# Performance work log

Hardware: AMD Instinct MI355X
Metric: run time of the kernel (lower is better)

Reference implementation:

```python
import jax, jax.numpy as jnp
import numpy as np

N_NODES = 50000

def _gcn_conv(x, W, b, src, dst, n):
    # GCNConv: add self-loops, symmetric normalization D^-1/2 (A+I) D^-1/2, then aggregate X@W
    h = x @ W  # [N, out]
    loop = jnp.arange(n, dtype=src.dtype)
    s = jnp.concatenate([src, loop])
    d = jnp.concatenate([dst, loop])
    deg = jax.ops.segment_sum(jnp.ones_like(d, dtype=h.dtype), d, num_segments=n)  # in-degree incl self-loop (>=1)
    dinv = jax.lax.rsqrt(deg)
    norm = dinv[s] * dinv[d]  # [E+N]
    msg = h[s] * norm[:, None]  # gather + scale
    out = jax.ops.segment_sum(msg, d, num_segments=n)  # scatter-add
    return out + b

def setup_inputs() -> dict:
    key = jax.random.key(0)
    k1, k2, k3, k4, k5 = jax.random.split(key, 5)
    F_IN, HID, CLS, E = 256, 128, 32, 800000
    x = jax.random.normal(k1, (N_NODES, F_IN), dtype=jnp.float32)
    edge_index = jax.random.randint(k2, (2, E), 0, N_NODES, dtype=jnp.int64)
    W1 = jax.random.normal(k3, (F_IN, HID), dtype=jnp.float32) / np.sqrt(F_IN)
    b1 = jnp.zeros((HID,), dtype=jnp.float32)
    W2 = jax.random.normal(k4, (HID, CLS), dtype=jnp.float32) / np.sqrt(HID)
    b2 = jnp.zeros((CLS,), dtype=jnp.float32)
    return {"x": x, "edge_index": edge_index, "W1": W1, "b1": b1, "W2": W2, "b2": b2}

def reference(x, edge_index, W1, b1, W2, b2):
    src, dst = edge_index[0], edge_index[1]
    h = _gcn_conv(x, W1, b1, src, dst, N_NODES)
    h = jax.nn.relu(h)
    h = _gcn_conv(h, W2, b2, src, dst, N_NODES)
    return jax.nn.log_softmax(h, axis=1)
```

## Files before the change

kernel.cpp:

```cpp
#include <hip/hip_runtime.h>

#define N_NODES 50000
#define N_PAD   50176
#define F_IN 256
#define HID 128
#define CLS 32
#define N_EDGE 800000

#define NB    196
#define NPART 196
#define CHUNK 4082

typedef short bf16x8 __attribute__((ext_vector_type(8)));
typedef short s16x8  __attribute__((ext_vector_type(8)));
typedef float f32x2  __attribute__((ext_vector_type(2)));
typedef float f32x4  __attribute__((ext_vector_type(4)));
typedef float f32x8  __attribute__((ext_vector_type(8)));

static __device__ inline short f2bf(float f) {
    union { float f; unsigned u; } v; v.f = f;
    unsigned r = v.u + 0x7FFFu + ((v.u >> 16) & 1u);
    return (short)(r >> 16);
}

static __device__ inline unsigned char f2fp8(float f) {
    return (unsigned char)(__builtin_amdgcn_cvt_pk_fp8_f32(f, f, 0, false) & 0xFF);
}


__global__ __launch_bounds__(256) void k_pre(const int* __restrict__ dst,
                                             int* __restrict__ counts,
                                             const float* __restrict__ W1,
                                             short* __restrict__ Wt,
                                             const float* __restrict__ W2,
                                             short* __restrict__ Wt2) {
    int blk = blockIdx.x, tid = threadIdx.x;
    if (blk < NB) {
        __shared__ int hist[NPART];
        if (tid < NPART) hist[tid] = 0;
        __syncthreads();
        int lo = blk * CHUNK, hi = min(lo + CHUNK, N_EDGE);
        for (int e = lo + tid; e < hi; e += 256)
            atomicAdd(&hist[dst[e] >> 8], 1);
        __syncthreads();
        if (tid < NPART) counts[blk * NPART + tid] = hist[tid];
    } else if (blk < NB + 128) {
        int idx = (blk - NB) * 256 + tid;
        int k = idx >> 7;
        int n = idx & 127;
        Wt[n * F_IN + k] = f2bf(W1[(size_t)k * HID + n]);
    } else {
        int idx = (blk - NB - 128) * 256 + tid;
        int k = idx >> 5;
        int n = idx & 31;
        Wt2[n * HID + k] = f2bf(W2[(size_t)k * CLS + n]);
    }
}


__global__ __launch_bounds__(256) void k_scanP1(const int* __restrict__ counts,
                                                int* __restrict__ base,
                                                int* __restrict__ ptot) {
    __shared__ int s[256];
    int tid = threadIdx.x, p = blockIdx.x;
    int v = (tid < NB) ? counts[tid * NPART + p] : 0;
    s[tid] = v;
    __syncthreads();
#pragma unroll
    for (int off = 1; off < 256; off <<= 1) {
        int t = (tid >= off) ? s[tid - off] : 0;
        __syncthreads();
        s[tid] += t;
        __syncthreads();
    }
    if (tid < NB) base[tid * NPART + p] = s[tid] - v;
    if (tid == 255) ptot[p] = s[255];
}


__global__ __launch_bounds__(256) void k_bucket(const int* __restrict__ src,
                                                const int* __restrict__ dst,
                                                const int* __restrict__ base,
                                                const int* __restrict__ ptot,
                                                int* __restrict__ bucket) {
    __shared__ int s[256];
    __shared__ int cur[NPART];
    int tid = threadIdx.x, blk = blockIdx.x;
    int v = (tid < NPART) ? ptot[tid] : 0;
    s[tid] = v;
    __syncthreads();
#pragma unroll
    for (int off = 1; off < 256; off <<= 1) {
        int t = (tid >= off) ? s[tid - off] : 0;
        __syncthreads();
        s[tid] += t;
        __syncthreads();
    }
    if (tid < NPART) cur[tid] = base[blk * NPART + tid] + (s[tid] - v);
    __syncthreads();
    int lo = blk * CHUNK, hi = min(lo + CHUNK, N_EDGE);
    for (int e = lo + tid; e < hi; e += 256) {
        int d = dst[e], sv = src[e];
        int pos = atomicAdd(&cur[d >> 8], 1);
        bucket[pos] = ((d & 255) << 16) | sv;
    }
}


__global__ __launch_bounds__(256) void k_csrf_gemm1(const int* __restrict__ bucket,
                                                    const int* __restrict__ ptot,
                                                    int* __restrict__ esrc,
                                                    int* __restrict__ offs,
                                                    float* __restrict__ dinv,
                                                    const float* __restrict__ x,
                                                    const short* __restrict__ Wt,
                                                    unsigned char* __restrict__ h) {
    int blk = blockIdx.x, tid = threadIdx.x;
    if (blk < NPART) {
        __shared__ int s[256], hist[256], cur[256];
        __shared__ int sbeg;
        int p = blk;
        int v = (tid < NPART) ? ptot[tid] : 0;
        s[tid] = v;
        __syncthreads();
#pragma unroll
        for (int off = 1; off < 256; off <<= 1) {
            int t = (tid >= off) ? s[tid - off] : 0;
            __syncthreads();
            s[tid] += t;
            __syncthreads();
        }
        if (tid == p) sbeg = s[tid] - v;
        hist[tid] = 0;
        __syncthreads();
        int beg = sbeg, end = sbeg + ptot[p];
        for (int i = beg + tid; i < end; i += 256)
            atomicAdd(&hist[bucket[i] >> 16], 1);
        __syncthreads();
        int hv = hist[tid];
        s[tid] = hv;
        __syncthreads();
#pragma unroll
        for (int off = 1; off < 256; off <<= 1) {
            int t = (tid >= off) ? s[tid - off] : 0;
            __syncthreads();
            s[tid] += t;
            __syncthreads();
        }
        int excl = s[tid] - hv;
        cur[tid] = excl;
        int node = p * 256 + tid;
        if (node <= N_NODES) offs[node] = beg + excl;
        if (node < N_NODES) dinv[node] = rsqrtf((float)(hv + 1));
        __syncthreads();
        for (int i = beg + tid; i < end; i += 256) {
            int pk = bucket[i];
            int slot = atomicAdd(&cur[pk >> 16], 1);
            esrc[beg + slot] = pk & 0xFFFF;
        }
        return;
    }

    const int gblk = blk - NPART;
    const int lane = tid & 63;
    const int w    = tid >> 6;
    const int l15  = lane & 15;
    const int lk   = lane >> 4;
    const int row0 = gblk * 128 + w * 32;

    f32x4 acc[2][8] = {};

#pragma unroll
    for (int ks = 0; ks < F_IN / 32; ++ks) {
        const int kbase = ks * 32 + lk * 8;

        bf16x8 afrag[2];
#pragma unroll
        for (int mt = 0; mt < 2; ++mt) {
            int row = row0 + mt * 16 + l15;
            row = min(row, N_NODES - 1);
            f32x8 xv = *(const f32x8*)(x + (size_t)row * F_IN + kbase);
            bf16x8 a;
#pragma unroll
            for (int e = 0; e < 8; ++e) a[e] = f2bf(xv[e]);
            afrag[mt] = a;
        }

        bf16x8 bfrag[8];
#pragma unroll
        for (int nt = 0; nt < 8; ++nt) {
            int col = nt * 16 + l15;
            bfrag[nt] = *(const bf16x8*)(Wt + (size_t)col * F_IN + kbase);
        }

#pragma unroll
        for (int mt = 0; mt < 2; ++mt)
#pragma unroll
            for (int nt = 0; nt < 8; ++nt)
                acc[mt][nt] = __builtin_amdgcn_mfma_f32_16x16x32_bf16(
                    afrag[mt], bfrag[nt], acc[mt][nt], 0, 0, 0);
    }

#pragma unroll
    for (int mt = 0; mt < 2; ++mt) {
#pragma unroll
        for (int r = 0; r < 4; ++r) {
            int m = row0 + mt * 16 + lk * 4 + r;
            if (m < N_NODES) {
#pragma unroll
                for (int nt = 0; nt < 8; ++nt) {
                    int n = nt * 16 + l15;
                    h[(size_t)m * HID + n] = f2fp8(acc[mt][nt][r]);
                }
            }
        }
    }
}


__global__ __launch_bounds__(256) void k_gather1(const int* __restrict__ offs,
                                                 const int* __restrict__ esrc,
                                                 const unsigned char* __restrict__ h,
                                                 const float* __restrict__ dinv,
                                                 const float* __restrict__ b,
                                                 short* __restrict__ out) {
    int node = blockIdx.x * 16 + (threadIdx.x >> 4);
    int lane = threadIdx.x & 15;
    if (node >= N_NODES) return;
    int f = lane * 8;
    float dv = dinv[node];
    uint2 hv = *(const uint2*)(h + (size_t)node * HID + f);
    f32x2 q0 = __builtin_amdgcn_cvt_pk_f32_fp8(hv.x, false);
    f32x2 q1 = __builtin_amdgcn_cvt_pk_f32_fp8(hv.x, true);
    f32x2 q2 = __builtin_amdgcn_cvt_pk_f32_fp8(hv.y, false);
    f32x2 q3 = __builtin_amdgcn_cvt_pk_f32_fp8(hv.y, true);
    float self = dv * dv;
    float a0 = q0[0] * self, a1 = q0[1] * self, a2 = q1[0] * self, a3 = q1[1] * self;
    float a4 = q2[0] * self, a5 = q2[1] * self, a6 = q3[0] * self, a7 = q3[1] * self;

    int beg = offs[node], end = offs[node + 1];
    int p = beg;
#define ACC8(vv, nn) { \
    f32x2 c0 = __builtin_amdgcn_cvt_pk_f32_fp8(vv.x, false); \
    f32x2 c1 = __builtin_amdgcn_cvt_pk_f32_fp8(vv.x, true);  \
    f32x2 c2 = __builtin_amdgcn_cvt_pk_f32_fp8(vv.y, false); \
    f32x2 c3 = __builtin_amdgcn_cvt_pk_f32_fp8(vv.y, true);  \
    a0 += c0[0] * nn; a1 += c0[1] * nn; a2 += c1[0] * nn; a3 += c1[1] * nn; \
    a4 += c2[0] * nn; a5 += c2[1] * nn; a6 += c3[0] * nn; a7 += c3[1] * nn; }
    for (; p + 7 < end; p += 8) {
        int s0 = esrc[p + 0], s1 = esrc[p + 1], s2 = esrc[p + 2], s3 = esrc[p + 3];
        int s4 = esrc[p + 4], s5 = esrc[p + 5], s6 = esrc[p + 6], s7 = esrc[p + 7];
        float n0 = dinv[s0] * dv, n1 = dinv[s1] * dv, n2 = dinv[s2] * dv, n3 = dinv[s3] * dv;
        float n4 = dinv[s4] * dv, n5 = dinv[s5] * dv, n6 = dinv[s6] * dv, n7 = dinv[s7] * dv;
        uint2 v0 = *(const uint2*)(h + (size_t)s0 * HID + f);
        uint2 v1 = *(const uint2*)(h + (size_t)s1 * HID + f);
        uint2 v2 = *(const uint2*)(h + (size_t)s2 * HID + f);
        uint2 v3 = *(const uint2*)(h + (size_t)s3 * HID + f);
        uint2 v4 = *(const uint2*)(h + (size_t)s4 * HID + f);
        uint2 v5 = *(const uint2*)(h + (size_t)s5 * HID + f);
        uint2 v6 = *(const uint2*)(h + (size_t)s6 * HID + f);
        uint2 v7 = *(const uint2*)(h + (size_t)s7 * HID + f);
        ACC8(v0, n0); ACC8(v1, n1); ACC8(v2, n2); ACC8(v3, n3);
        ACC8(v4, n4); ACC8(v5, n5); ACC8(v6, n6); ACC8(v7, n7);
    }
    for (; p + 3 < end; p += 4) {
        int s0 = esrc[p + 0], s1 = esrc[p + 1], s2 = esrc[p + 2], s3 = esrc[p + 3];
        float n0 = dinv[s0] * dv, n1 = dinv[s1] * dv, n2 = dinv[s2] * dv, n3 = dinv[s3] * dv;
        uint2 v0 = *(const uint2*)(h + (size_t)s0 * HID + f);
        uint2 v1 = *(const uint2*)(h + (size_t)s1 * HID + f);
        uint2 v2 = *(const uint2*)(h + (size_t)s2 * HID + f);
        uint2 v3 = *(const uint2*)(h + (size_t)s3 * HID + f);
        ACC8(v0, n0); ACC8(v1, n1); ACC8(v2, n2); ACC8(v3, n3);
    }
    for (; p < end; ++p) {
        int s = esrc[p];
        float nrm = dinv[s] * dv;
        uint2 v = *(const uint2*)(h + (size_t)s * HID + f);
        ACC8(v, nrm);
    }
#undef ACC8
    float4 bv0 = *(const float4*)(b + f);
    float4 bv1 = *(const float4*)(b + f + 4);
    s16x8 o = { f2bf(a0 + bv0.x), f2bf(a1 + bv0.y), f2bf(a2 + bv0.z), f2bf(a3 + bv0.w),
                f2bf(a4 + bv1.x), f2bf(a5 + bv1.y), f2bf(a6 + bv1.z), f2bf(a7 + bv1.w) };
    *(s16x8*)(out + (size_t)node * HID + f) = o;
}


__global__ __launch_bounds__(256) void k_gemm2_mfma(const short* __restrict__ a,
                                                    const short* __restrict__ Wt,
                                                    unsigned char* __restrict__ h) {
    const int lane = threadIdx.x & 63;
    const int w    = threadIdx.x >> 6;
    const int l15  = lane & 15;
    const int lk   = lane >> 4;
    const int row0 = blockIdx.x * 128 + w * 32;

    f32x4 acc[2][2] = {};

#pragma unroll
    for (int ks = 0; ks < HID / 32; ++ks) {
        const int kbase = ks * 32 + lk * 8;

        bf16x8 afrag[2];
#pragma unroll
        for (int mt = 0; mt < 2; ++mt) {
            int row = row0 + mt * 16 + l15;
            row = min(row, N_NODES - 1);
            bf16x8 av = *(const bf16x8*)(a + (size_t)row * HID + kbase);
#pragma unroll
            for (int e = 0; e < 8; ++e) if (av[e] < 0) av[e] = 0;
            afrag[mt] = av;
        }

        bf16x8 bfrag[2];
#pragma unroll
        for (int nt = 0; nt < 2; ++nt) {
            int col = nt * 16 + l15;
            bfrag[nt] = *(const bf16x8*)(Wt + (size_t)col * HID + kbase);
        }

#pragma unroll
        for (int mt = 0; mt < 2; ++mt)
#pragma unroll
            for (int nt = 0; nt < 2; ++nt)
                acc[mt][nt] = __builtin_amdgcn_mfma_f32_16x16x32_bf16(
                    afrag[mt], bfrag[nt], acc[mt][nt], 0, 0, 0);
    }

#pragma unroll
    for (int mt = 0; mt < 2; ++mt) {
#pragma unroll
        for (int r = 0; r < 4; ++r) {
            int m = row0 + mt * 16 + lk * 4 + r;
            if (m < N_NODES) {
#pragma unroll
                for (int nt = 0; nt < 2; ++nt) {
                    int n = nt * 16 + l15;
                    h[(size_t)m * CLS + n] = f2fp8(acc[mt][nt][r]);
                }
            }
        }
    }
}


__global__ __launch_bounds__(256) void k_gather2(const int* __restrict__ offs,
                                                 const int* __restrict__ esrc,
                                                 const unsigned char* __restrict__ h,
                                                 const float* __restrict__ dinv,
                                                 const float* __restrict__ b,
                                                 float* __restrict__ out) {
    int node = blockIdx.x * 32 + (threadIdx.x >> 3);
    int sub = threadIdx.x & 7;
    if (node >= N_NODES) return;
    int f = sub * 4;
    float dv = dinv[node];
    unsigned hv = *(const unsigned*)(h + (size_t)node * CLS + f);
    f32x2 hlo = __builtin_amdgcn_cvt_pk_f32_fp8(hv, false);
    f32x2 hhi = __builtin_amdgcn_cvt_pk_f32_fp8(hv, true);
    float self = dv * dv;
    float a0 = hlo[0] * self, a1 = hlo[1] * self, a2 = hhi[0] * self, a3 = hhi[1] * self;
    int beg = offs[node], end = offs[node + 1];
    int p = beg;
#define ACC4(vv, nn) { \
    f32x2 l = __builtin_amdgcn_cvt_pk_f32_fp8(vv, false); \
    f32x2 u = __builtin_amdgcn_cvt_pk_f32_fp8(vv, true);  \
    a0 += l[0] * nn; a1 += l[1] * nn; a2 += u[0] * nn; a3 += u[1] * nn; }
    for (; p + 7 < end; p += 8) {
        int s0 = esrc[p], s1 = esrc[p + 1], s2 = esrc[p + 2], s3 = esrc[p + 3];
        int s4 = esrc[p + 4], s5 = esrc[p + 5], s6 = esrc[p + 6], s7 = esrc[p + 7];
        float n0 = dinv[s0] * dv, n1 = dinv[s1] * dv, n2 = dinv[s2] * dv, n3 = dinv[s3] * dv;
        float n4 = dinv[s4] * dv, n5 = dinv[s5] * dv, n6 = dinv[s6] * dv, n7 = dinv[s7] * dv;
        unsigned v0 = *(const unsigned*)(h + (size_t)s0 * CLS + f);
        unsigned v1 = *(const unsigned*)(h + (size_t)s1 * CLS + f);
        unsigned v2 = *(const unsigned*)(h + (size_t)s2 * CLS + f);
        unsigned v3 = *(const unsigned*)(h + (size_t)s3 * CLS + f);
        unsigned v4 = *(const unsigned*)(h + (size_t)s4 * CLS + f);
        unsigned v5 = *(const unsigned*)(h + (size_t)s5 * CLS + f);
        unsigned v6 = *(const unsigned*)(h + (size_t)s6 * CLS + f);
        unsigned v7 = *(const unsigned*)(h + (size_t)s7 * CLS + f);
        ACC4(v0, n0); ACC4(v1, n1); ACC4(v2, n2); ACC4(v3, n3);
        ACC4(v4, n4); ACC4(v5, n5); ACC4(v6, n6); ACC4(v7, n7);
    }
    for (; p + 3 < end; p += 4) {
        int s0 = esrc[p], s1 = esrc[p + 1], s2 = esrc[p + 2], s3 = esrc[p + 3];
        float n0 = dinv[s0] * dv, n1 = dinv[s1] * dv, n2 = dinv[s2] * dv, n3 = dinv[s3] * dv;
        unsigned v0 = *(const unsigned*)(h + (size_t)s0 * CLS + f);
        unsigned v1 = *(const unsigned*)(h + (size_t)s1 * CLS + f);
        unsigned v2 = *(const unsigned*)(h + (size_t)s2 * CLS + f);
        unsigned v3 = *(const unsigned*)(h + (size_t)s3 * CLS + f);
        ACC4(v0, n0); ACC4(v1, n1); ACC4(v2, n2); ACC4(v3, n3);
    }
    for (; p < end; ++p) {
        int s = esrc[p];
        float nrm = dinv[s] * dv;
        unsigned v = *(const unsigned*)(h + (size_t)s * CLS + f);
        ACC4(v, nrm);
    }
#undef ACC4
    float4 bv = *(const float4*)(b + f);
    float4 acc = { a0 + bv.x, a1 + bv.y, a2 + bv.z, a3 + bv.w };

    float m = fmaxf(fmaxf(acc.x, acc.y), fmaxf(acc.z, acc.w));
    m = fmaxf(m, __shfl_xor(m, 1, 8));
    m = fmaxf(m, __shfl_xor(m, 2, 8));
    m = fmaxf(m, __shfl_xor(m, 4, 8));
    float sum = expf(acc.x - m) + expf(acc.y - m) + expf(acc.z - m) + expf(acc.w - m);
    sum += __shfl_xor(sum, 1, 8);
    sum += __shfl_xor(sum, 2, 8);
    sum += __shfl_xor(sum, 4, 8);
    float l = m + logf(sum);
    float4 o = { acc.x - l, acc.y - l, acc.z - l, acc.w - l };
    *(float4*)(out + (size_t)node * CLS + f) = o;
}


extern "C" void kernel_launch(void* const* d_in, const int* in_sizes, int n_in,
                              void* d_out, int out_size, void* d_ws, size_t ws_size,
                              hipStream_t stream) {
    const float* x  = (const float*)d_in[0];
    const int*   ei = (const int*)d_in[1];
    const float* W1 = (const float*)d_in[2];
    const float* b1 = (const float*)d_in[3];
    const float* W2 = (const float*)d_in[4];
    const float* b2 = (const float*)d_in[5];
    float* out = (float*)d_out;

    const int* src = ei;
    const int* dst = ei + N_EDGE;

    int* counts   = (int*)d_ws;
    int* base     = counts + NB * NPART;
    int* ptot     = base + NB * NPART;
    int* bucket   = ptot + 256;
    int* offs     = bucket + N_EDGE;
    int* esrc     = offs + N_PAD;
    float* dinv   = (float*)(esrc + N_EDGE);
    unsigned char* h1 = (unsigned char*)(dinv + N_PAD);
    short* a1     = (short*)(h1 + (size_t)N_NODES * HID);
    unsigned char* h2 = (unsigned char*)(a1 + (size_t)N_NODES * HID);
    short* Wt     = (short*)(h2 + (size_t)N_NODES * CLS);
    short* Wt2    = Wt + HID * F_IN;

    k_pre       <<<NB + 128 + 16, 256, 0, stream>>>(dst, counts, W1, Wt, W2, Wt2);
    k_scanP1    <<<NPART,         256, 0, stream>>>(counts, base, ptot);
    k_bucket    <<<NB,            256, 0, stream>>>(src, dst, base, ptot, bucket);
    k_csrf_gemm1<<<NPART + 391,   256, 0, stream>>>(bucket, ptot, esrc, offs, dinv, x, Wt, h1);

    k_gather1   <<<3125,          256, 0, stream>>>(offs, esrc, h1, dinv, b1, a1);
    k_gemm2_mfma<<<391,           256, 0, stream>>>(a1, Wt2, h2);
    k_gather2   <<<1563,          256, 0, stream>>>(offs, esrc, h2, dinv, b2, out);
}
```

Measured before the change: 92.18 us.

## Co-schedule GEMM1 with edge bucketing and shrink GEMM tile to 64 rows

The first feature GEMM now runs in the same launch as the edge-bucketing step instead of alongside the CSR finalization, and CSR finalization becomes its own kernel. The intent is to hide the long bucketing scatter behind GEMM work, with a lighter CSR kernel afterward. The GEMM tile also drops from 128 to 64 rows per block (782 blocks), which cuts register use and spreads the work over more blocks. The cost is that each B fragment is reused across fewer rows, so W is reloaded more often.

Result: slower. 105.5 us (+14.4%).

```diff
diff --git a/kernel.cpp b/kernel.cpp
--- a/kernel.cpp
+++ b/kernel.cpp
@@ -10,6 +10,7 @@
 #define NB    196
 #define NPART 196
 #define CHUNK 4082
+#define GBLKS 782
 
 typedef short bf16x8 __attribute__((ext_vector_type(8)));
 typedef short s16x8  __attribute__((ext_vector_type(8)));
@@ -78,48 +79,18 @@
 }
 
 
-__global__ __launch_bounds__(256) void k_bucket(const int* __restrict__ src,
-                                                const int* __restrict__ dst,
-                                                const int* __restrict__ base,
-                                                const int* __restrict__ ptot,
-                                                int* __restrict__ bucket) {
-    __shared__ int s[256];
-    __shared__ int cur[NPART];
-    int tid = threadIdx.x, blk = blockIdx.x;
-    int v = (tid < NPART) ? ptot[tid] : 0;
-    s[tid] = v;
-    __syncthreads();
-#pragma unroll
-    for (int off = 1; off < 256; off <<= 1) {
-        int t = (tid >= off) ? s[tid - off] : 0;
-        __syncthreads();
-        s[tid] += t;
-        __syncthreads();
-    }
-    if (tid < NPART) cur[tid] = base[blk * NPART + tid] + (s[tid] - v);
-    __syncthreads();
-    int lo = blk * CHUNK, hi = min(lo + CHUNK, N_EDGE);
-    for (int e = lo + tid; e < hi; e += 256) {
-        int d = dst[e], sv = src[e];
-        int pos = atomicAdd(&cur[d >> 8], 1);
-        bucket[pos] = ((d & 255) << 16) | sv;
-    }
-}
-
-
-__global__ __launch_bounds__(256) void k_csrf_gemm1(const int* __restrict__ bucket,
-                                                    const int* __restrict__ ptot,
-                                                    int* __restrict__ esrc,
-                                                    int* __restrict__ offs,
-                                                    float* __restrict__ dinv,
-                                                    const float* __restrict__ x,
-                                                    const short* __restrict__ Wt,
-                                                    unsigned char* __restrict__ h) {
+__global__ __launch_bounds__(256) void k_bucket_gemm1(const int* __restrict__ src,
+                                                      const int* __restrict__ dst,
+                                                      const int* __restrict__ base,
+                                                      const int* __restrict__ ptot,
+                                                      int* __restrict__ bucket,
+                                                      const float* __restrict__ x,
+                                                      const short* __restrict__ Wt,
+                                                      unsigned char* __restrict__ h) {
     int blk = blockIdx.x, tid = threadIdx.x;
-    if (blk < NPART) {
-        __shared__ int s[256], hist[256], cur[256];
-        __shared__ int sbeg;
-        int p = blk;
+    if (blk < NB) {
+        __shared__ int s[256];
+        __shared__ int cur[NPART];
         int v = (tid < NPART) ? ptot[tid] : 0;
         s[tid] = v;
         __syncthreads();
@@ -130,61 +101,35 @@
             s[tid] += t;
             __syncthreads();
         }
-        if (tid == p) sbeg = s[tid] - v;
-        hist[tid] = 0;
-        __syncthreads();
-        int beg = sbeg, end = sbeg + ptot[p];
-        for (int i = beg + tid; i < end; i += 256)
-            atomicAdd(&hist[bucket[i] >> 16], 1);
-        __syncthreads();
-        int hv = hist[tid];
-        s[tid] = hv;
-        __syncthreads();
-#pragma unroll
-        for (int off = 1; off < 256; off <<= 1) {
-            int t = (tid >= off) ? s[tid - off] : 0;
-            __syncthreads();
-            s[tid] += t;
-            __syncthreads();
-        }
-        int excl = s[tid] - hv;
-        cur[tid] = excl;
-        int node = p * 256 + tid;
-        if (node <= N_NODES) offs[node] = beg + excl;
-        if (node < N_NODES) dinv[node] = rsqrtf((float)(hv + 1));
-        __syncthreads();
-        for (int i = beg + tid; i < end; i += 256) {
-            int pk = bucket[i];
-            int slot = atomicAdd(&cur[pk >> 16], 1);
-            esrc[beg + slot] = pk & 0xFFFF;
+        if (tid < NPART) cur[tid] = base[blk * NPART + tid] + (s[tid] - v);
+        __syncthreads();
+        int lo = blk * CHUNK, hi = min(lo + CHUNK, N_EDGE);
+        for (int e = lo + tid; e < hi; e += 256) {
+            int d = dst[e], sv = src[e];
+            int pos = atomicAdd(&cur[d >> 8], 1);
+            bucket[pos] = ((d & 255) << 16) | sv;
         }
         return;
     }
 
-    const int gblk = blk - NPART;
+    const int gblk = blk - NB;
     const int lane = tid & 63;
     const int w    = tid >> 6;
     const int l15  = lane & 15;
     const int lk   = lane >> 4;
-    const int row0 = gblk * 128 + w * 32;
-
-    f32x4 acc[2][8] = {};
+    const int row0 = gblk * 64 + w * 16;
+
+    f32x4 acc[8] = {};
 
 #pragma unroll
     for (int ks = 0; ks < F_IN / 32; ++ks) {
         const int kbase = ks * 32 + lk * 8;
 
-        bf16x8 afrag[2];
-#pragma unroll
-        for (int mt = 0; mt < 2; ++mt) {
-            int row = row0 + mt * 16 + l15;
-            row = min(row, N_NODES - 1);
-            f32x8 xv = *(const f32x8*)(x + (size_t)row * F_IN + kbase);
-            bf16x8 a;
-#pragma unroll
-            for (int e = 0; e < 8; ++e) a[e] = f2bf(xv[e]);
-            afrag[mt] = a;
-        }
+        int row = min(row0 + l15, N_NODES - 1);
+        f32x8 xv = *(const f32x8*)(x + (size_t)row * F_IN + kbase);
+        bf16x8 afrag;
+#pragma unroll
+        for (int e = 0; e < 8; ++e) afrag[e] = f2bf(xv[e]);
 
         bf16x8 bfrag[8];
 #pragma unroll
@@ -194,26 +139,69 @@
         }
 
 #pragma unroll
-        for (int mt = 0; mt < 2; ++mt)
-#pragma unroll
-            for (int nt = 0; nt < 8; ++nt)
-                acc[mt][nt] = __builtin_amdgcn_mfma_f32_16x16x32_bf16(
-                    afrag[mt], bfrag[nt], acc[mt][nt], 0, 0, 0);
-    }
-
-#pragma unroll
-    for (int mt = 0; mt < 2; ++mt) {
-#pragma unroll
-        for (int r = 0; r < 4; ++r) {
-            int m = row0 + mt * 16 + lk * 4 + r;
-            if (m < N_NODES) {
-#pragma unroll
-                for (int nt = 0; nt < 8; ++nt) {
-                    int n = nt * 16 + l15;
-                    h[(size_t)m * HID + n] = f2fp8(acc[mt][nt][r]);
-                }
+        for (int nt = 0; nt < 8; ++nt)
+            acc[nt] = __builtin_amdgcn_mfma_f32_16x16x32_bf16(afrag, bfrag[nt], acc[nt], 0, 0, 0);
+    }
+
+#pragma unroll
+    for (int r = 0; r < 4; ++r) {
+        int m = row0 + lk * 4 + r;
+        if (m < N_NODES) {
+#pragma unroll
+            for (int nt = 0; nt < 8; ++nt) {
+                int n = nt * 16 + l15;
+                h[(size_t)m * HID + n] = f2fp8(acc[nt][r]);
             }
         }
+    }
+}
+
+
+__global__ __launch_bounds__(256) void k_csr_final(const int* __restrict__ bucket,
+                                                   const int* __restrict__ ptot,
+                                                   int* __restrict__ esrc,
+                                                   int* __restrict__ offs,
+                                                   float* __restrict__ dinv) {
+    __shared__ int s[256], hist[256], cur[256];
+    __shared__ int sbeg;
+    int tid = threadIdx.x, p = blockIdx.x;
+    int v = (tid < NPART) ? ptot[tid] : 0;
+    s[tid] = v;
+    __syncthreads();
+#pragma unroll
+    for (int off = 1; off < 256; off <<= 1) {
+        int t = (tid >= off) ? s[tid - off] : 0;
+        __syncthreads();
+        s[tid] += t;
+        __syncthreads();
+    }
+    if (tid == p) sbeg = s[tid] - v;
+    hist[tid] = 0;
+    __syncthreads();
+    int beg = sbeg, end = sbeg + ptot[p];
+    for (int i = beg + tid; i < end; i += 256)
+        atomicAdd(&hist[bucket[i] >> 16], 1);
+    __syncthreads();
+    int hv = hist[tid];
+    s[tid] = hv;
+    __syncthreads();
+#pragma unroll
+    for (int off = 1; off < 256; off <<= 1) {
+        int t = (tid >= off) ? s[tid - off] : 0;
+        __syncthreads();
+        s[tid] += t;
+        __syncthreads();
+    }
+    int excl = s[tid] - hv;
+    cur[tid] = excl;
+    int node = p * 256 + tid;
+    if (node <= N_NODES) offs[node] = beg + excl;
+    if (node < N_NODES) dinv[node] = rsqrtf((float)(hv + 1));
+    __syncthreads();
+    for (int i = beg + tid; i < end; i += 256) {
+        int pk = bucket[i];
+        int slot = atomicAdd(&cur[pk >> 16], 1);
+        esrc[beg + slot] = pk & 0xFFFF;
     }
 }
 
@@ -443,12 +431,12 @@
     short* Wt     = (short*)(h2 + (size_t)N_NODES * CLS);
     short* Wt2    = Wt + HID * F_IN;
 
-    k_pre       <<<NB + 128 + 16, 256, 0, stream>>>(dst, counts, W1, Wt, W2, Wt2);
-    k_scanP1    <<<NPART,         256, 0, stream>>>(counts, base, ptot);
-    k_bucket    <<<NB,            256, 0, stream>>>(src, dst, base, ptot, bucket);
-    k_csrf_gemm1<<<NPART + 391,   256, 0, stream>>>(bucket, ptot, esrc, offs, dinv, x, Wt, h1);
-
-    k_gather1   <<<3125,          256, 0, stream>>>(offs, esrc, h1, dinv, b1, a1);
-    k_gemm2_mfma<<<391,           256, 0, stream>>>(a1, Wt2, h2);
-    k_gather2   <<<1563,          256, 0, stream>>>(offs, esrc, h2, dinv, b2, out);
-}
+    k_pre         <<<NB + 128 + 16, 256, 0, stream>>>(dst, counts, W1, Wt, W2, Wt2);
+    k_scanP1      <<<NPART,         256, 0, stream>>>(counts, base, ptot);
+    k_bucket_gemm1<<<NB + GBLKS,    256, 0, stream>>>(src, dst, base, ptot, bucket, x, Wt, h1);
+    k_csr_final   <<<NPART,         256, 0, stream>>>(bucket, ptot, esrc, offs, dinv);
+
+    k_gather1     <<<3125,          256, 0, stream>>>(offs, esrc, h1, dinv, b1, a1);
+    k_gemm2_mfma  <<<391,           256, 0, stream>>>(a1, Wt2, h2);
+    k_gather2     <<<1563,          256, 0, stream>>>(offs, esrc, h2, dinv, b2, out);
+}
```

## Stage X tile through swizzled LDS and halve rows per GEMM1 block

Applied to the files above, without the earlier changes.

The GEMM1 part of the fused CSR/GEMM kernel now loads a 64-row tile of x into shared memory with coalesced float4 loads, converts it to bf16, and stores it with an XOR swizzle. MFMA A-fragments are then read from LDS. Each wave now handles 16 rows instead of 32, so the grid doubles to 782 GEMM blocks for more parallelism. The cost is a 32KB LDS allocation for every block, including the CSR blocks that reuse it, which can lower occupancy. Each W fragment is also reused across fewer rows, so more B loads happen per output.

Result: slower. 101.0 us (+9.6%).

```diff
diff --git a/kernel.cpp b/kernel.cpp
--- a/kernel.cpp
+++ b/kernel.cpp
@@ -10,12 +10,13 @@
 #define NB    196
 #define NPART 196
 #define CHUNK 4082
+#define GBLKS 782
 
 typedef short bf16x8 __attribute__((ext_vector_type(8)));
+typedef short s16x4  __attribute__((ext_vector_type(4)));
 typedef short s16x8  __attribute__((ext_vector_type(8)));
 typedef float f32x2  __attribute__((ext_vector_type(2)));
 typedef float f32x4  __attribute__((ext_vector_type(4)));
-typedef float f32x8  __attribute__((ext_vector_type(8)));
 
 static __device__ inline short f2bf(float f) {
     union { float f; unsigned u; } v; v.f = f;
@@ -115,76 +116,86 @@
                                                     const float* __restrict__ x,
                                                     const short* __restrict__ Wt,
                                                     unsigned char* __restrict__ h) {
+    __shared__ short tile[64][256];
     int blk = blockIdx.x, tid = threadIdx.x;
+
     if (blk < NPART) {
-        __shared__ int s[256], hist[256], cur[256];
-        __shared__ int sbeg;
+        int* sA = (int*)&tile[0][0];
+        int* sB = sA + 256;
+        int* sC = sB + 256;
+        int* sX = sC + 256;
         int p = blk;
         int v = (tid < NPART) ? ptot[tid] : 0;
-        s[tid] = v;
+        sA[tid] = v;
         __syncthreads();
 #pragma unroll
         for (int off = 1; off < 256; off <<= 1) {
-            int t = (tid >= off) ? s[tid - off] : 0;
+            int t = (tid >= off) ? sA[tid - off] : 0;
             __syncthreads();
-            s[tid] += t;
+            sA[tid] += t;
             __syncthreads();
         }
-        if (tid == p) sbeg = s[tid] - v;
-        hist[tid] = 0;
-        __syncthreads();
-        int beg = sbeg, end = sbeg + ptot[p];
+        if (tid == p) sX[0] = sA[tid] - v;
+        sB[tid] = 0;
+        __syncthreads();
+        int beg = sX[0], end = beg + ptot[p];
         for (int i = beg + tid; i < end; i += 256)
-            atomicAdd(&hist[bucket[i] >> 16], 1);
-        __syncthreads();
-        int hv = hist[tid];
-        s[tid] = hv;
+            atomicAdd(&sB[bucket[i] >> 16], 1);
+        __syncthreads();
+        int hv = sB[tid];
+        sA[tid] = hv;
         __syncthreads();
 #pragma unroll
         for (int off = 1; off < 256; off <<= 1) {
-            int t = (tid >= off) ? s[tid - off] : 0;
+            int t = (tid >= off) ? sA[tid - off] : 0;
             __syncthreads();
-            s[tid] += t;
+            sA[tid] += t;
             __syncthreads();
         }
-        int excl = s[tid] - hv;
-        cur[tid] = excl;
+        int excl = sA[tid] - hv;
+        sC[tid] = excl;
         int node = p * 256 + tid;
         if (node <= N_NODES) offs[node] = beg + excl;
         if (node < N_NODES) dinv[node] = rsqrtf((float)(hv + 1));
         __syncthreads();
         for (int i = beg + tid; i < end; i += 256) {
             int pk = bucket[i];
-            int slot = atomicAdd(&cur[pk >> 16], 1);
+            int slot = atomicAdd(&sC[pk >> 16], 1);
             esrc[beg + slot] = pk & 0xFFFF;
         }
         return;
     }
 
-    const int gblk = blk - NPART;
+    const int R0 = (blk - NPART) * 64;
+
+#pragma unroll 8
+    for (int it = 0; it < 16; ++it) {
+        int rl = it * 4 + (tid >> 6);
+        int row = min(R0 + rl, N_NODES - 1);
+        int c = (tid & 63) * 4;
+        f32x4 xv = *(const f32x4*)(x + (size_t)row * F_IN + c);
+        s16x4 bv = { f2bf(xv[0]), f2bf(xv[1]), f2bf(xv[2]), f2bf(xv[3]) };
+        int byte = rl * 512 + c * 2;
+        byte ^= ((rl & 7) << 4);
+        *(s16x4*)((char*)&tile[0][0] + byte) = bv;
+    }
+    __syncthreads();
+
     const int lane = tid & 63;
     const int w    = tid >> 6;
     const int l15  = lane & 15;
     const int lk   = lane >> 4;
-    const int row0 = gblk * 128 + w * 32;
-
-    f32x4 acc[2][8] = {};
+
+    f32x4 acc[8] = {};
 
 #pragma unroll
     for (int ks = 0; ks < F_IN / 32; ++ks) {
         const int kbase = ks * 32 + lk * 8;
 
-        bf16x8 afrag[2];
-#pragma unroll
-        for (int mt = 0; mt < 2; ++mt) {
-            int row = row0 + mt * 16 + l15;
-            row = min(row, N_NODES - 1);
-            f32x8 xv = *(const f32x8*)(x + (size_t)row * F_IN + kbase);
-            bf16x8 a;
-#pragma unroll
-            for (int e = 0; e < 8; ++e) a[e] = f2bf(xv[e]);
-            afrag[mt] = a;
-        }
+        int rl = w * 16 + l15;
+        int byte = rl * 512 + kbase * 2;
+        byte ^= ((rl & 7) << 4);
+        bf16x8 afrag = *(const bf16x8*)((char*)&tile[0][0] + byte);
 
         bf16x8 bfrag[8];
 #pragma unroll
@@ -194,24 +205,18 @@
         }
 
 #pragma unroll
-        for (int mt = 0; mt < 2; ++mt)
-#pragma unroll
-            for (int nt = 0; nt < 8; ++nt)
-                acc[mt][nt] = __builtin_amdgcn_mfma_f32_16x16x32_bf16(
-                    afrag[mt], bfrag[nt], acc[mt][nt], 0, 0, 0);
-    }
-
-#pragma unroll
-    for (int mt = 0; mt < 2; ++mt) {
-#pragma unroll
-        for (int r = 0; r < 4; ++r) {
-            int m = row0 + mt * 16 + lk * 4 + r;
-            if (m < N_NODES) {
-#pragma unroll
-                for (int nt = 0; nt < 8; ++nt) {
-                    int n = nt * 16 + l15;
-                    h[(size_t)m * HID + n] = f2fp8(acc[mt][nt][r]);
-                }
+        for (int nt = 0; nt < 8; ++nt)
+            acc[nt] = __builtin_amdgcn_mfma_f32_16x16x32_bf16(afrag, bfrag[nt], acc[nt], 0, 0, 0);
+    }
+
+#pragma unroll
+    for (int r = 0; r < 4; ++r) {
+        int m = R0 + w * 16 + lk * 4 + r;
+        if (m < N_NODES) {
+#pragma unroll
+            for (int nt = 0; nt < 8; ++nt) {
+                int n = nt * 16 + l15;
+                h[(size_t)m * HID + n] = f2fp8(acc[nt][r]);
             }
         }
     }
@@ -446,7 +451,7 @@
     k_pre       <<<NB + 128 + 16, 256, 0, stream>>>(dst, counts, W1, Wt, W2, Wt2);
     k_scanP1    <<<NPART,         256, 0, stream>>>(counts, base, ptot);
     k_bucket    <<<NB,            256, 0, stream>>>(src, dst, base, ptot, bucket);
-    k_csrf_gemm1<<<NPART + 391,   256, 0, stream>>>(bucket, ptot, esrc, offs, dinv, x, Wt, h1);
+    k_csrf_gemm1<<<NPART + GBLKS, 256, 0, stream>>>(bucket, ptot, esrc, offs, dinv, x, Wt, h1);
 
     k_gather1   <<<3125,          256, 0, stream>>>(offs, esrc, h1, dinv, b1, a1);
     k_gemm2_mfma<<<391,           256, 0, stream>>>(a1, Wt2, h2);
```
